# Performance work log

Measured on AMD Instinct MI355X. Metric: run time of the kernel, lower is better.

The kernel has to match this reference:

```python
import jax, jax.numpy as jnp
import numpy as np

RHO = 1060.0   # blood density kg/m^3
DX = 1e-3      # grid spacing
CCFL = 0.9     # CFL number
EPS_A = 1e-6   # area floor


def setup_inputs() -> dict:
    key = jax.random.key(0)
    k0, k1, k2 = jax.random.split(key, 3)
    M = 90000          # 3 vessels x 30000 cells
    T = 150            # time steps
    Rs = jax.random.normal(k0, (4,), dtype=jnp.float32)
    sim_dat = jnp.ones((2, M), dtype=jnp.float32)            # row0: A, row1: Q seed
    sim_dat_const = jax.random.uniform(k1, (11, M), dtype=jnp.float32)
    input_data = jax.random.uniform(k2, (T,), dtype=jnp.float32)
    strides = jnp.array([[0, 30000], [30000, 60000], [60000, 90000]], dtype=jnp.int32)
    return {"Rs": Rs, "sim_dat": sim_dat, "sim_dat_const": sim_dat_const,
            "input_data": input_data, "strides": strides, "upper": T}


def reference(Rs, sim_dat, sim_dat_const, input_data, strides, upper):
    M = sim_dat.shape[1]
    # --- SimDense: softplus reparam of 4 resistance scale factors ---
    rs = jax.nn.softplus(Rs)
    idx = jnp.arange(M)
    m1 = (idx >= strides[1, 0]) & (idx < strides[1, 1])  # vessel 1 region
    m2 = (idx >= strides[2, 0]) & (idx < strides[2, 1])  # vessel 2 region
    # constant rows (shifted positive)
    A0 = sim_dat_const[0] + 0.5     # reference area
    beta = sim_dat_const[1] + 1.0   # wall stiffness
    R1 = sim_dat_const[7] + 0.5     # proximal resistance (VAR_INDEX_1)
    R2 = sim_dat_const[8] + 0.5     # distal resistance (VAR_INDEX_2)
    # scatter scaled resistances into vessel-1 / vessel-2 regions
    R1 = jnp.where(m1, rs[0] * R1, jnp.where(m2, rs[2] * R1, R1))
    R2 = jnp.where(m1, rs[1] * R2, jnp.where(m2, rs[3] * R2, R2))
    Rtot = R1 + R2

    A_init = sim_dat[0]
    Q_init = 0.1 * sim_dat[1]
    starts = strides[:, 0]
    ends = strides[:, 1] - 1
    mids = (strides[:, 0] + strides[:, 1]) // 2

    def step(carry, inflow):
        A, Q = carry
        A = jnp.maximum(A, EPS_A)
        sq = jnp.sqrt(A / A0)
        P = beta * (sq - 1.0)                 # tube-law pressure
        u = Q / A
        c = jnp.sqrt(0.5 * beta / RHO * sq)   # wave speed
        smax = jnp.max(jnp.abs(u) + c)
        dt = CCFL * DX / smax                 # CFL-limited timestep
        # conservative fluxes for (A, Q)
        F_A = Q
        F_Q = Q * u + beta / (3.0 * RHO * A0) * A * sq
        # Lax-Friedrichs interface fluxes
        fhA = 0.5 * (F_A[:-1] + F_A[1:]) - 0.5 * smax * (A[1:] - A[:-1])
        fhQ = 0.5 * (F_Q[:-1] + F_Q[1:]) - 0.5 * smax * (Q[1:] - Q[:-1])
        lam = dt / DX
        A_new = A.at[1:-1].add(-lam * (fhA[1:] - fhA[:-1]))
        Q_new = Q.at[1:-1].add(-lam * (fhQ[1:] - fhQ[:-1]))
        # inlet / junction BC: prescribed inflow at each vessel start
        Q_new = Q_new.at[starts].set(inflow)
        # outlet BC: resistive Windkessel Q = P / (R1 + R2)
        Q_new = Q_new.at[ends].set(P[ends] / Rtot[ends])
        A_new = jnp.maximum(A_new, EPS_A)
        return (A_new, Q_new), P[mids]          # record mid-vessel pressures

    _, p = jax.lax.scan(step, (A_init, Q_init), input_data)
    return p  # [upper, 3]
```

## Files before the change

kernel.cpp:

```cpp
#include <hip/hip_runtime.h>

static constexpr int MM  = 90000;
static constexpr int TT  = 150;
static constexpr int BS  = 256;
static constexpr int CPT = 4;
static constexpr int CPB = BS * CPT;
static constexpr int NB  = (MM + CPB - 1) / CPB;
static constexpr int WPB = BS / 64;
static constexpr int NWAVE  = NB * WPB;
static constexpr int WPAGES = 384;
static constexpr int PAGE_U32 = 2048;
static constexpr int PAGE_U64 = 1024;

__device__ unsigned int       g_wmax[WPAGES][PAGE_U32];
__device__ unsigned long long g_edge_s[NB][PAGE_U64];
__device__ unsigned long long g_dummy64;

__device__ __forceinline__ float softplus_f(float x) {
    return fmaxf(x, 0.0f) + log1pf(expf(-fabsf(x)));
}
__device__ __forceinline__ unsigned long long packAQ(float A, float Q) {
    return ((unsigned long long)__float_as_uint(Q) << 32) | (unsigned long long)__float_as_uint(A);
}
#define AG_LOAD32(p)     __hip_atomic_load((p), __ATOMIC_RELAXED, __HIP_MEMORY_SCOPE_AGENT)
#define AG_LOAD64(p)     __hip_atomic_load((p), __ATOMIC_RELAXED, __HIP_MEMORY_SCOPE_AGENT)
#define AG_STORE32(p, v) __hip_atomic_store((p), (v), __ATOMIC_RELAXED, __HIP_MEMORY_SCOPE_AGENT)
#define AG_STORE64(p, v) __hip_atomic_store((p), (v), __ATOMIC_RELAXED, __HIP_MEMORY_SCOPE_AGENT)

#define DPP_MAX(x, ctrl, rm, bm)                                                     \
    x = fmaxf(x, __int_as_float(__builtin_amdgcn_update_dpp(                          \
                     0, __float_as_int(x), (ctrl), (rm), (bm), true)))
__device__ __forceinline__ float wave_max64(float x) {
    DPP_MAX(x, 0x111, 0xf, 0xf);
    DPP_MAX(x, 0x112, 0xf, 0xf);
    DPP_MAX(x, 0x114, 0xf, 0xe);
    DPP_MAX(x, 0x118, 0xf, 0xc);
    DPP_MAX(x, 0x142, 0xa, 0xf);
    DPP_MAX(x, 0x143, 0xc, 0xf);
    return x;
}

__global__ void init_ws_kernel() {
    int i = blockIdx.x * blockDim.x + threadIdx.x;
    int stride = gridDim.x * blockDim.x;
    unsigned int* pw = &g_wmax[0][0];
    for (int j = i; j < WPAGES * PAGE_U32; j += stride)
        pw[j] = ((j / PAGE_U32) < NWAVE) ? 0u : 1u;
    unsigned long long* pe = &g_edge_s[0][0];
    for (int j = i; j < NB * PAGE_U64; j += stride) pe[j] = 0ull;
    if (i == 0) g_dummy64 = ~0ull;
}

__global__ void __launch_bounds__(BS) sim_kernel(
    const float* __restrict__ Rs,
    const float* __restrict__ sim_dat,
    const float* __restrict__ sdc,
    const float* __restrict__ inflow,
    float* __restrict__ out)
{
    __shared__ float sE[2][WPB][2][3];
    __shared__ float s_bc[2];
    __shared__ float s_hL[3], s_hR[3];
    __shared__ float s_inflow[TT];

    const int b    = blockIdx.x;
    const int tid  = threadIdx.x;
    const int wv   = tid >> 6;
    const int lane = tid & 63;
    const int base = b * CPB + tid * CPT;
    const int gw   = b * WPB + wv;

    for (int j = tid; j < TT; j += BS) s_inflow[j] = inflow[j];

    float A[CPT], Q[CPT], A0v[CPT], bet[CPT], cbv[CPT], k2v[CPT], sq[CPT], FQ[CPT];
    bool  act[CPT];
    #pragma unroll
    for (int c = 0; c < CPT; ++c) {
        int i = base + c;
        act[c] = (i < MM);
        if (act[c]) {
            A[c]   = fmaxf(sim_dat[i], 1e-6f);
            Q[c]   = 0.1f * sim_dat[MM + i];
            A0v[c] = sdc[i] + 0.5f;
            bet[c] = sdc[MM + i] + 1.0f;
        } else { A[c] = 1.0f; Q[c] = 0.0f; A0v[c] = 1.0f; bet[c] = 1.0f; }
        cbv[c] = (0.5f * bet[c]) / 1060.0f;
        k2v[c] = bet[c] / (3180.0f * A0v[c]);
    }
    const bool isStart = (base == 0) | (base == 30000) | (base == 60000);
    const bool isEnd   = (base + 3 == 29999) | (base + 3 == 59999) | (base + 3 == 89999);
    const int midSlot = (base == 15000) ? 0 : (base == 45000) ? 1 : (base == 75000) ? 2 : -1;
    float Rtot = 1.0f;
    if (isEnd) {
        int i3 = base + 3;
        float R1 = sdc[7 * MM + i3] + 0.5f;
        float R2 = sdc[8 * MM + i3] + 0.5f;
        if (i3 == 59999)      { R1 *= softplus_f(Rs[0]); R2 *= softplus_f(Rs[1]); }
        else if (i3 == 89999) { R1 *= softplus_f(Rs[2]); R2 *= softplus_f(Rs[3]); }
        Rtot = R1 + R2;
    }

    const bool pubL = (tid == 0) && (b > 0);
    const bool pubR = (tid == BS - 1) && (b < NB - 1);

    const unsigned int* pwl = &g_wmax[lane][0];

    float s4 = 0.0f;
    #pragma unroll
    for (int c = 0; c < CPT; ++c) {
        sq[c] = sqrtf(A[c] / A0v[c]);
        float uu = Q[c] / A[c];
        float cc = sqrtf(cbv[c] * sq[c]);
        FQ[c] = Q[c] * uu + k2v[c] * A[c] * sq[c];
        s4 = fmaxf(s4, act[c] ? (fabsf(uu) + cc) : 0.0f);
    }
    if (pubL) {
        AG_STORE64(&g_edge_s[b][0], packAQ(A[0], Q[0]));
        AG_STORE64(&g_edge_s[b][1], (unsigned long long)__float_as_uint(FQ[0]));
    }
    if (pubR) {
        AG_STORE64(&g_edge_s[b][2], packAQ(A[3], Q[3]));
        AG_STORE64(&g_edge_s[b][3], (unsigned long long)__float_as_uint(FQ[3]));
    }
    {
        float red = wave_max64(s4);
        if (lane == 63) AG_STORE32(&g_wmax[gw][0], __float_as_uint(red));
    }
    if (lane == 0)       { sE[0][wv][0][0] = A[0]; sE[0][wv][0][1] = Q[0]; sE[0][wv][0][2] = FQ[0]; }
    else if (lane == 63) { sE[0][wv][1][0] = A[3]; sE[0][wv][1][1] = Q[3]; sE[0][wv][1][2] = FQ[3]; }

    for (int t = 0; t < TT; ++t) {
        const int par = t & 1, npar = par ^ 1;

        unsigned int x0, x1, x2, x3, x4, x5;
        unsigned long long e64;
        const unsigned long long* pE = &g_dummy64;
        if (wv == 0) {
            const int t4 = t * 4;
            if (lane == 0 && b > 0)           pE = &g_edge_s[b - 1][t4 + 2];
            else if (lane == 1 && b > 0)      pE = &g_edge_s[b - 1][t4 + 3];
            else if (lane == 2 && b < NB - 1) pE = &g_edge_s[b + 1][t4 + 0];
            else if (lane == 3 && b < NB - 1) pE = &g_edge_s[b + 1][t4 + 1];
            const unsigned int* p = pwl + t;
            x0 = AG_LOAD32(p);
            x1 = AG_LOAD32(p +  64 * PAGE_U32);
            x2 = AG_LOAD32(p + 128 * PAGE_U32);
            x3 = AG_LOAD32(p + 192 * PAGE_U32);
            x4 = AG_LOAD32(p + 256 * PAGE_U32);
            x5 = AG_LOAD32(p + 320 * PAGE_U32);
            e64 = AG_LOAD64(pE);
        }

        float Am = __shfl_up(A[3], 1, 64),  Qm = __shfl_up(Q[3], 1, 64),  Fm = __shfl_up(FQ[3], 1, 64);
        float Ap = __shfl_down(A[0], 1, 64), Qp = __shfl_down(Q[0], 1, 64), Fp = __shfl_down(FQ[0], 1, 64);

        float dFA[CPT], lapA[CPT], dFQ[CPT], lapQ[CPT];
        #pragma unroll
        for (int c = 0; c < CPT; ++c) {
            float Al = (c == 0) ? Am : A[c-1],  Ql = (c == 0) ? Qm : Q[c-1],  Fl = (c == 0) ? Fm : FQ[c-1];
            float Ar = (c == 3) ? Ap : A[c+1],  Qr = (c == 3) ? Qp : Q[c+1],  Fr = (c == 3) ? Fp : FQ[c+1];
            dFA[c]  = 0.5f * (Qr - Ql);
            lapA[c] = 0.5f * (Ar - 2.0f * A[c] + Al);
            dFQ[c]  = 0.5f * (Fr - Fl);
            lapQ[c] = 0.5f * (Qr - 2.0f * Q[c] + Ql);
        }
        if (midSlot >= 0) out[t * 3 + midSlot] = bet[0] * (sq[0] - 1.0f);
        float qFix = 0.0f;
        if (isStart) qFix = s_inflow[t];
        if (isEnd)   qFix = (bet[3] * (sq[3] - 1.0f)) / Rtot;

        if (wv == 0) {
            const unsigned int* p = pwl + t;
            bool ok = __all((x0 != 0u) & (x1 != 0u) & (x2 != 0u) & (x3 != 0u) &
                            (x4 != 0u) & (x5 != 0u) & (e64 != 0ull));
            while (!ok) {
                x0 = AG_LOAD32(p);
                x1 = AG_LOAD32(p +  64 * PAGE_U32);
                x2 = AG_LOAD32(p + 128 * PAGE_U32);
                x3 = AG_LOAD32(p + 192 * PAGE_U32);
                x4 = AG_LOAD32(p + 256 * PAGE_U32);
                x5 = AG_LOAD32(p + 320 * PAGE_U32);
                e64 = AG_LOAD64(pE);
                ok = __all((x0 != 0u) & (x1 != 0u) & (x2 != 0u) & (x3 != 0u) &
                           (x4 != 0u) & (x5 != 0u) & (e64 != 0ull));
            }
            if (lane == 0 && b > 0)           { s_hL[0] = __uint_as_float((unsigned int)e64);
                                                s_hL[1] = __uint_as_float((unsigned int)(e64 >> 32)); }
            else if (lane == 1 && b > 0)      { s_hL[2] = __uint_as_float((unsigned int)e64); }
            else if (lane == 2 && b < NB - 1) { s_hR[0] = __uint_as_float((unsigned int)e64);
                                                s_hR[1] = __uint_as_float((unsigned int)(e64 >> 32)); }
            else if (lane == 3 && b < NB - 1) { s_hR[2] = __uint_as_float((unsigned int)e64); }
            float m = fmaxf(fmaxf(fmaxf(__uint_as_float(x0), __uint_as_float(x1)),
                                  fmaxf(__uint_as_float(x2), __uint_as_float(x3))),
                            fmaxf(__uint_as_float(x4), __uint_as_float(x5)));
            m = wave_max64(m);
            const float smax = __int_as_float(__builtin_amdgcn_readlane(__float_as_int(m), 63));
            const float dt  = ((float)(0.9 * 0.001)) / smax;
            const float lam = dt / 0.001f;
            const float w   = lam * smax;
            if (lane == 0) { s_bc[0] = lam; s_bc[1] = w; }
        }
        __syncthreads();
        const float lam = s_bc[0];
        const float w   = s_bc[1];

        if (lane == 0 && (wv > 0 || b > 0)) {
            float Al, Ql, Fl;
            if (wv > 0) { Al = sE[par][wv-1][1][0]; Ql = sE[par][wv-1][1][1]; Fl = sE[par][wv-1][1][2]; }
            else        { Al = s_hL[0];             Ql = s_hL[1];             Fl = s_hL[2]; }
            dFA[0]  = 0.5f * (Q[1] - Ql);
            lapA[0] = 0.5f * (A[1] - 2.0f * A[0] + Al);
            dFQ[0]  = 0.5f * (FQ[1] - Fl);
            lapQ[0] = 0.5f * (Q[1] - 2.0f * Q[0] + Ql);
        }
        if (lane == 63 && (wv < WPB - 1 || b < NB - 1)) {
            float Ar, Qr, Fr;
            if (wv < WPB - 1) { Ar = sE[par][wv+1][0][0]; Qr = sE[par][wv+1][0][1]; Fr = sE[par][wv+1][0][2]; }
            else              { Ar = s_hR[0];             Qr = s_hR[1];             Fr = s_hR[2]; }
            dFA[3]  = 0.5f * (Qr - Q[2]);
            lapA[3] = 0.5f * (Ar - 2.0f * A[3] + A[2]);
            dFQ[3]  = 0.5f * (Fr - FQ[2]);
            lapQ[3] = 0.5f * (Qr - 2.0f * Q[3] + Q[2]);
        }

        #pragma unroll
        for (int c = 0; c < CPT; ++c) {
            int i = base + c;
            if (act[c] && i > 0 && i < MM - 1) {
                A[c] = fmaf(w, lapA[c], fmaf(-lam, dFA[c], A[c]));
                Q[c] = fmaf(w, lapQ[c], fmaf(-lam, dFQ[c], Q[c]));
            }
        }
        if (isStart) Q[0] = qFix;
        if (isEnd)   Q[3] = qFix;
        #pragma unroll
        for (int c = 0; c < CPT; ++c) A[c] = fmaxf(A[c], 1e-6f);

        const int n4 = (t + 1) * 4;
        if (pubL) AG_STORE64(&g_edge_s[b][n4 + 0], packAQ(A[0], Q[0]));
        if (pubR) AG_STORE64(&g_edge_s[b][n4 + 2], packAQ(A[3], Q[3]));

        float uu[CPT];
        s4 = 0.0f;
        #pragma unroll
        for (int c = 0; c < CPT; ++c) {
            sq[c] = sqrtf(A[c] / A0v[c]);
            uu[c] = Q[c] / A[c];
            float cc = sqrtf(cbv[c] * sq[c]);
            s4 = fmaxf(s4, act[c] ? (fabsf(uu[c]) + cc) : 0.0f);
        }
        {
            float red = wave_max64(s4);
            if (lane == 63) AG_STORE32(&g_wmax[gw][t + 1], __float_as_uint(red));
        }
        #pragma unroll
        for (int c = 0; c < CPT; ++c)
            FQ[c] = Q[c] * uu[c] + k2v[c] * A[c] * sq[c];

        if (pubL) AG_STORE64(&g_edge_s[b][n4 + 1], (unsigned long long)__float_as_uint(FQ[0]));
        if (pubR) AG_STORE64(&g_edge_s[b][n4 + 3], (unsigned long long)__float_as_uint(FQ[3]));

        if (lane == 0)       { sE[npar][wv][0][0] = A[0]; sE[npar][wv][0][1] = Q[0]; sE[npar][wv][0][2] = FQ[0]; }
        else if (lane == 63) { sE[npar][wv][1][0] = A[3]; sE[npar][wv][1][1] = Q[3]; sE[npar][wv][1][2] = FQ[3]; }
    }
}

extern "C" void kernel_launch(void* const* d_in, const int* in_sizes, int n_in,
                              void* d_out, int out_size, void* d_ws, size_t ws_size,
                              hipStream_t stream) {
    (void)in_sizes; (void)n_in; (void)d_ws; (void)ws_size; (void)out_size;

    const float* Rs      = (const float*)d_in[0];
    const float* sim_dat = (const float*)d_in[1];
    const float* sdc     = (const float*)d_in[2];
    const float* inflow  = (const float*)d_in[3];
    float* out = (float*)d_out;

    hipLaunchKernelGGL(init_ws_kernel, dim3(240), dim3(256), 0, stream);

    hipLaunchKernelGGL(sim_kernel, dim3(NB), dim3(BS), 0, stream,
                       Rs, sim_dat, sdc, inflow, out);
}
```

Baseline: 459.9 us.

## Replace block barrier with LDS flag broadcast and pack halo edges into dwordx4

```diff
diff --git a/kernel.cpp b/kernel.cpp
--- a/kernel.cpp
+++ b/kernel.cpp
@@ -7,28 +7,59 @@
 static constexpr int CPB = BS * CPT;
 static constexpr int NB  = (MM + CPB - 1) / CPB;
 static constexpr int WPB = BS / 64;
-static constexpr int NWAVE  = NB * WPB;
+static constexpr int NWAVE = NB * WPB;
 static constexpr int WPAGES = 384;
 static constexpr int PAGE_U32 = 2048;
-static constexpr int PAGE_U64 = 1024;
-
-__device__ unsigned int       g_wmax[WPAGES][PAGE_U32];
-__device__ unsigned long long g_edge_s[NB][PAGE_U64];
-__device__ unsigned long long g_dummy64;
+static constexpr int DUMMY_OFF = 1024;
+
+typedef unsigned int u32x4 __attribute__((ext_vector_type(4)));
+
+__device__ __attribute__((aligned(128))) unsigned int g_wmax[WPAGES][PAGE_U32];
+__device__ __attribute__((aligned(128))) unsigned int g_edge[NB][PAGE_U32];
 
 __device__ __forceinline__ float softplus_f(float x) {
     return fmaxf(x, 0.0f) + log1pf(expf(-fabsf(x)));
 }
-__device__ __forceinline__ unsigned long long packAQ(float A, float Q) {
-    return ((unsigned long long)__float_as_uint(Q) << 32) | (unsigned long long)__float_as_uint(A);
-}
-#define AG_LOAD32(p)     __hip_atomic_load((p), __ATOMIC_RELAXED, __HIP_MEMORY_SCOPE_AGENT)
-#define AG_LOAD64(p)     __hip_atomic_load((p), __ATOMIC_RELAXED, __HIP_MEMORY_SCOPE_AGENT)
 #define AG_STORE32(p, v) __hip_atomic_store((p), (v), __ATOMIC_RELAXED, __HIP_MEMORY_SCOPE_AGENT)
-#define AG_STORE64(p, v) __hip_atomic_store((p), (v), __ATOMIC_RELAXED, __HIP_MEMORY_SCOPE_AGENT)
-
-#define DPP_MAX(x, ctrl, rm, bm)                                                     \
-    x = fmaxf(x, __int_as_float(__builtin_amdgcn_update_dpp(                          \
+
+#define ISSUE7(x0,x1,x2,x3,x4,x5,h,p0,p1,p2,p3,p4,p5,ph)                        \
+    asm volatile("global_load_dword %0, %7, off sc1\n\t"                        \
+                 "global_load_dword %1, %8, off sc1\n\t"                        \
+                 "global_load_dword %2, %9, off sc1\n\t"                        \
+                 "global_load_dword %3, %10, off sc1\n\t"                       \
+                 "global_load_dword %4, %11, off sc1\n\t"                       \
+                 "global_load_dword %5, %12, off sc1\n\t"                       \
+                 "global_load_dwordx4 %6, %13, off sc1"                         \
+                 : "=&v"(x0),"=&v"(x1),"=&v"(x2),"=&v"(x3),"=&v"(x4),"=&v"(x5),"=&v"(h) \
+                 : "v"(p0),"v"(p1),"v"(p2),"v"(p3),"v"(p4),"v"(p5),"v"(ph)      \
+                 : "memory")
+#define POLL7(x0,x1,x2,x3,x4,x5,h,p0,p1,p2,p3,p4,p5,ph)                         \
+    asm volatile("global_load_dword %0, %7, off sc1\n\t"                        \
+                 "global_load_dword %1, %8, off sc1\n\t"                        \
+                 "global_load_dword %2, %9, off sc1\n\t"                        \
+                 "global_load_dword %3, %10, off sc1\n\t"                       \
+                 "global_load_dword %4, %11, off sc1\n\t"                       \
+                 "global_load_dword %5, %12, off sc1\n\t"                       \
+                 "global_load_dwordx4 %6, %13, off sc1\n\t"                     \
+                 "s_waitcnt vmcnt(0)"                                           \
+                 : "=&v"(x0),"=&v"(x1),"=&v"(x2),"=&v"(x3),"=&v"(x4),"=&v"(x5),"=&v"(h) \
+                 : "v"(p0),"v"(p1),"v"(p2),"v"(p3),"v"(p4),"v"(p5),"v"(ph)      \
+                 : "memory")
+#define ISSUE1(h, ph)                                                           \
+    asm volatile("global_load_dwordx4 %0, %1, off sc1"                          \
+                 : "=&v"(h) : "v"(ph) : "memory")
+#define POLL1(h, ph)                                                            \
+    asm volatile("global_load_dwordx4 %0, %1, off sc1\n\t"                      \
+                 "s_waitcnt vmcnt(0)"                                           \
+                 : "=&v"(h) : "v"(ph) : "memory")
+#define WAITVM()  do { asm volatile("s_waitcnt vmcnt(0)" ::: "memory");         \
+                       __builtin_amdgcn_sched_barrier(0); } while (0)
+#define FENCE_LDS() asm volatile("s_waitcnt lgkmcnt(0)" ::: "memory")
+#define STORE_X4(p, v)                                                          \
+    asm volatile("global_store_dwordx4 %0, %1, off sc1" :: "v"(p), "v"(v) : "memory")
+
+#define DPP_MAX(x, ctrl, rm, bm)                                                \
+    x = fmaxf(x, __int_as_float(__builtin_amdgcn_update_dpp(                    \
                      0, __float_as_int(x), (ctrl), (rm), (bm), true)))
 __device__ __forceinline__ float wave_max64(float x) {
     DPP_MAX(x, 0x111, 0xf, 0xf);
@@ -45,10 +76,9 @@
     int stride = gridDim.x * blockDim.x;
     unsigned int* pw = &g_wmax[0][0];
     for (int j = i; j < WPAGES * PAGE_U32; j += stride)
-        pw[j] = ((j / PAGE_U32) < NWAVE) ? 0u : 1u;
-    unsigned long long* pe = &g_edge_s[0][0];
-    for (int j = i; j < NB * PAGE_U64; j += stride) pe[j] = 0ull;
-    if (i == 0) g_dummy64 = ~0ull;
+        pw[j] = (((j >> 11) < NWAVE) && ((j & (PAGE_U32 - 1)) < DUMMY_OFF)) ? 0u : 1u;
+    unsigned int* pe = &g_edge[0][0];
+    for (int j = i; j < NB * PAGE_U32; j += stride) pe[j] = 0u;
 }
 
 __global__ void __launch_bounds__(BS) sim_kernel(
@@ -59,8 +89,7 @@
     float* __restrict__ out)
 {
     __shared__ float sE[2][WPB][2][3];
-    __shared__ float s_bc[2];
-    __shared__ float s_hL[3], s_hR[3];
+    __shared__ unsigned long long s_lamw[TT];
     __shared__ float s_inflow[TT];
 
     const int b    = blockIdx.x;
@@ -70,7 +99,7 @@
     const int base = b * CPB + tid * CPT;
     const int gw   = b * WPB + wv;
 
-    for (int j = tid; j < TT; j += BS) s_inflow[j] = inflow[j];
+    for (int j = tid; j < TT; j += BS) { s_inflow[j] = inflow[j]; s_lamw[j] = 0ull; }
 
     float A[CPT], Q[CPT], A0v[CPT], bet[CPT], cbv[CPT], k2v[CPT], sq[CPT], FQ[CPT];
     bool  act[CPT];
@@ -103,8 +132,6 @@
     const bool pubL = (tid == 0) && (b > 0);
     const bool pubR = (tid == BS - 1) && (b < NB - 1);
 
-    const unsigned int* pwl = &g_wmax[lane][0];
-
     float s4 = 0.0f;
     #pragma unroll
     for (int c = 0; c < CPT; ++c) {
@@ -114,41 +141,36 @@
         FQ[c] = Q[c] * uu + k2v[c] * A[c] * sq[c];
         s4 = fmaxf(s4, act[c] ? (fabsf(uu) + cc) : 0.0f);
     }
-    if (pubL) {
-        AG_STORE64(&g_edge_s[b][0], packAQ(A[0], Q[0]));
-        AG_STORE64(&g_edge_s[b][1], (unsigned long long)__float_as_uint(FQ[0]));
-    }
-    if (pubR) {
-        AG_STORE64(&g_edge_s[b][2], packAQ(A[3], Q[3]));
-        AG_STORE64(&g_edge_s[b][3], (unsigned long long)__float_as_uint(FQ[3]));
-    }
+    if (pubL) { u32x4 ev = { __float_as_uint(A[0]), __float_as_uint(Q[0]), __float_as_uint(FQ[0]), 0u };
+                STORE_X4(&g_edge[b][0], ev); }
+    if (pubR) { u32x4 ev = { __float_as_uint(A[3]), __float_as_uint(Q[3]), __float_as_uint(FQ[3]), 0u };
+                STORE_X4(&g_edge[b][4], ev); }
+    if (lane == 0)       { sE[0][wv][0][0] = A[0]; sE[0][wv][0][1] = Q[0]; sE[0][wv][0][2] = FQ[0]; }
+    else if (lane == 63) { sE[0][wv][1][0] = A[3]; sE[0][wv][1][1] = Q[3]; sE[0][wv][1][2] = FQ[3]; }
     {
         float red = wave_max64(s4);
+        FENCE_LDS();
         if (lane == 63) AG_STORE32(&g_wmax[gw][0], __float_as_uint(red));
     }
-    if (lane == 0)       { sE[0][wv][0][0] = A[0]; sE[0][wv][0][1] = Q[0]; sE[0][wv][0][2] = FQ[0]; }
-    else if (lane == 63) { sE[0][wv][1][0] = A[3]; sE[0][wv][1][1] = Q[3]; sE[0][wv][1][2] = FQ[3]; }
+    __syncthreads();
 
     for (int t = 0; t < TT; ++t) {
         const int par = t & 1, npar = par ^ 1;
 
         unsigned int x0, x1, x2, x3, x4, x5;
-        unsigned long long e64;
-        const unsigned long long* pE = &g_dummy64;
+        u32x4 h;
+        const unsigned int *p0, *p1, *p2, *p3, *p4, *p5, *ph;
         if (wv == 0) {
-            const int t4 = t * 4;
-            if (lane == 0 && b > 0)           pE = &g_edge_s[b - 1][t4 + 2];
-            else if (lane == 1 && b > 0)      pE = &g_edge_s[b - 1][t4 + 3];
-            else if (lane == 2 && b < NB - 1) pE = &g_edge_s[b + 1][t4 + 0];
-            else if (lane == 3 && b < NB - 1) pE = &g_edge_s[b + 1][t4 + 1];
-            const unsigned int* p = pwl + t;
-            x0 = AG_LOAD32(p);
-            x1 = AG_LOAD32(p +  64 * PAGE_U32);
-            x2 = AG_LOAD32(p + 128 * PAGE_U32);
-            x3 = AG_LOAD32(p + 192 * PAGE_U32);
-            x4 = AG_LOAD32(p + 256 * PAGE_U32);
-            x5 = AG_LOAD32(p + 320 * PAGE_U32);
-            e64 = AG_LOAD64(pE);
+            p0 = &g_wmax[lane      ][t];  p1 = &g_wmax[lane +  64][t];
+            p2 = &g_wmax[lane + 128][t];  p3 = &g_wmax[lane + 192][t];
+            p4 = &g_wmax[lane + 256][t];  p5 = &g_wmax[lane + 320][t];
+            ph = (lane == 0 && b > 0) ? &g_edge[b - 1][t * 8 + 4]
+                                      : &g_wmax[lane][DUMMY_OFF];
+            ISSUE7(x0, x1, x2, x3, x4, x5, h, p0, p1, p2, p3, p4, p5, ph);
+        } else if (wv == WPB - 1) {
+            ph = (lane == 63 && b < NB - 1) ? &g_edge[b + 1][t * 8]
+                                            : &g_wmax[lane][DUMMY_OFF];
+            ISSUE1(h, ph);
         }
 
         float Am = __shfl_up(A[3], 1, 64),  Qm = __shfl_up(Q[3], 1, 64),  Fm = __shfl_up(FQ[3], 1, 64);
@@ -164,50 +186,51 @@
             dFQ[c]  = 0.5f * (Fr - Fl);
             lapQ[c] = 0.5f * (Qr - 2.0f * Q[c] + Ql);
         }
-        if (midSlot >= 0) out[t * 3 + midSlot] = bet[0] * (sq[0] - 1.0f);
         float qFix = 0.0f;
         if (isStart) qFix = s_inflow[t];
         if (isEnd)   qFix = (bet[3] * (sq[3] - 1.0f)) / Rtot;
-
+        const float Pmid = bet[0] * (sq[0] - 1.0f);
+
+        float lam, w;
+        float hA = 0.0f, hQ = 0.0f, hF = 0.0f;
         if (wv == 0) {
-            const unsigned int* p = pwl + t;
-            bool ok = __all((x0 != 0u) & (x1 != 0u) & (x2 != 0u) & (x3 != 0u) &
-                            (x4 != 0u) & (x5 != 0u) & (e64 != 0ull));
-            while (!ok) {
-                x0 = AG_LOAD32(p);
-                x1 = AG_LOAD32(p +  64 * PAGE_U32);
-                x2 = AG_LOAD32(p + 128 * PAGE_U32);
-                x3 = AG_LOAD32(p + 192 * PAGE_U32);
-                x4 = AG_LOAD32(p + 256 * PAGE_U32);
-                x5 = AG_LOAD32(p + 320 * PAGE_U32);
-                e64 = AG_LOAD64(pE);
-                ok = __all((x0 != 0u) & (x1 != 0u) & (x2 != 0u) & (x3 != 0u) &
-                           (x4 != 0u) & (x5 != 0u) & (e64 != 0ull));
+            WAITVM();
+            while (!__all((x0 != 0u) & (x1 != 0u) & (x2 != 0u) & (x3 != 0u) &
+                          (x4 != 0u) & (x5 != 0u) & (h.x != 0u) & (h.z != 0u))) {
+                POLL7(x0, x1, x2, x3, x4, x5, h, p0, p1, p2, p3, p4, p5, ph);
             }
-            if (lane == 0 && b > 0)           { s_hL[0] = __uint_as_float((unsigned int)e64);
-                                                s_hL[1] = __uint_as_float((unsigned int)(e64 >> 32)); }
-            else if (lane == 1 && b > 0)      { s_hL[2] = __uint_as_float((unsigned int)e64); }
-            else if (lane == 2 && b < NB - 1) { s_hR[0] = __uint_as_float((unsigned int)e64);
-                                                s_hR[1] = __uint_as_float((unsigned int)(e64 >> 32)); }
-            else if (lane == 3 && b < NB - 1) { s_hR[2] = __uint_as_float((unsigned int)e64); }
+            hA = __uint_as_float(h.x); hQ = __uint_as_float(h.y); hF = __uint_as_float(h.z);
             float m = fmaxf(fmaxf(fmaxf(__uint_as_float(x0), __uint_as_float(x1)),
                                   fmaxf(__uint_as_float(x2), __uint_as_float(x3))),
                             fmaxf(__uint_as_float(x4), __uint_as_float(x5)));
             m = wave_max64(m);
             const float smax = __int_as_float(__builtin_amdgcn_readlane(__float_as_int(m), 63));
-            const float dt  = ((float)(0.9 * 0.001)) / smax;
-            const float lam = dt / 0.001f;
-            const float w   = lam * smax;
-            if (lane == 0) { s_bc[0] = lam; s_bc[1] = w; }
-        }
-        __syncthreads();
-        const float lam = s_bc[0];
-        const float w   = s_bc[1];
+            const float dt = ((float)(0.9 * 0.001)) / smax;
+            lam = dt / 0.001f;
+            w   = lam * smax;
+            if (lane == 0) {
+                unsigned long long v = ((unsigned long long)__float_as_uint(w) << 32)
+                                       | (unsigned long long)__float_as_uint(lam);
+                __hip_atomic_store(&s_lamw[t], v, __ATOMIC_RELEASE, __HIP_MEMORY_SCOPE_WORKGROUP);
+            }
+        } else {
+            if (wv == WPB - 1) {
+                WAITVM();
+                while (!__all((h.x != 0u) & (h.z != 0u))) { POLL1(h, ph); }
+                hA = __uint_as_float(h.x); hQ = __uint_as_float(h.y); hF = __uint_as_float(h.z);
+            }
+            unsigned long long lw;
+            do {
+                lw = __hip_atomic_load(&s_lamw[t], __ATOMIC_ACQUIRE, __HIP_MEMORY_SCOPE_WORKGROUP);
+            } while ((unsigned int)lw == 0u);
+            lam = __uint_as_float((unsigned int)lw);
+            w   = __uint_as_float((unsigned int)(lw >> 32));
+        }
 
         if (lane == 0 && (wv > 0 || b > 0)) {
             float Al, Ql, Fl;
             if (wv > 0) { Al = sE[par][wv-1][1][0]; Ql = sE[par][wv-1][1][1]; Fl = sE[par][wv-1][1][2]; }
-            else        { Al = s_hL[0];             Ql = s_hL[1];             Fl = s_hL[2]; }
+            else        { Al = hA;                  Ql = hQ;                  Fl = hF; }
             dFA[0]  = 0.5f * (Q[1] - Ql);
             lapA[0] = 0.5f * (A[1] - 2.0f * A[0] + Al);
             dFQ[0]  = 0.5f * (FQ[1] - Fl);
@@ -216,7 +239,7 @@
         if (lane == 63 && (wv < WPB - 1 || b < NB - 1)) {
             float Ar, Qr, Fr;
             if (wv < WPB - 1) { Ar = sE[par][wv+1][0][0]; Qr = sE[par][wv+1][0][1]; Fr = sE[par][wv+1][0][2]; }
-            else              { Ar = s_hR[0];             Qr = s_hR[1];             Fr = s_hR[2]; }
+            else              { Ar = hA;                  Qr = hQ;                  Fr = hF; }
             dFA[3]  = 0.5f * (Qr - Q[2]);
             lapA[3] = 0.5f * (Ar - 2.0f * A[3] + A[2]);
             dFQ[3]  = 0.5f * (Fr - FQ[2]);
@@ -235,10 +258,7 @@
         if (isEnd)   Q[3] = qFix;
         #pragma unroll
         for (int c = 0; c < CPT; ++c) A[c] = fmaxf(A[c], 1e-6f);
-
-        const int n4 = (t + 1) * 4;
-        if (pubL) AG_STORE64(&g_edge_s[b][n4 + 0], packAQ(A[0], Q[0]));
-        if (pubR) AG_STORE64(&g_edge_s[b][n4 + 2], packAQ(A[3], Q[3]));
+        if (midSlot >= 0) out[t * 3 + midSlot] = Pmid;
 
         float uu[CPT];
         s4 = 0.0f;
@@ -249,19 +269,23 @@
             float cc = sqrtf(cbv[c] * sq[c]);
             s4 = fmaxf(s4, act[c] ? (fabsf(uu[c]) + cc) : 0.0f);
         }
+        #pragma unroll
+        for (int c = 0; c < CPT; ++c)
+            FQ[c] = Q[c] * uu[c] + k2v[c] * A[c] * sq[c];
+
+        const int n8 = (t + 1) * 8;
+        if (pubL) { u32x4 ev = { __float_as_uint(A[0]), __float_as_uint(Q[0]), __float_as_uint(FQ[0]), 0u };
+                    STORE_X4(&g_edge[b][n8], ev); }
+        if (pubR) { u32x4 ev = { __float_as_uint(A[3]), __float_as_uint(Q[3]), __float_as_uint(FQ[3]), 0u };
+                    STORE_X4(&g_edge[b][n8 + 4], ev); }
+
+        if (lane == 0)       { sE[npar][wv][0][0] = A[0]; sE[npar][wv][0][1] = Q[0]; sE[npar][wv][0][2] = FQ[0]; }
+        else if (lane == 63) { sE[npar][wv][1][0] = A[3]; sE[npar][wv][1][1] = Q[3]; sE[npar][wv][1][2] = FQ[3]; }
         {
             float red = wave_max64(s4);
+            FENCE_LDS();
             if (lane == 63) AG_STORE32(&g_wmax[gw][t + 1], __float_as_uint(red));
         }
-        #pragma unroll
-        for (int c = 0; c < CPT; ++c)
-            FQ[c] = Q[c] * uu[c] + k2v[c] * A[c] * sq[c];
-
-        if (pubL) AG_STORE64(&g_edge_s[b][n4 + 1], (unsigned long long)__float_as_uint(FQ[0]));
-        if (pubR) AG_STORE64(&g_edge_s[b][n4 + 3], (unsigned long long)__float_as_uint(FQ[3]));
-
-        if (lane == 0)       { sE[npar][wv][0][0] = A[0]; sE[npar][wv][0][1] = Q[0]; sE[npar][wv][0][2] = FQ[0]; }
-        else if (lane == 63) { sE[npar][wv][1][0] = A[3]; sE[npar][wv][1][1] = Q[3]; sE[npar][wv][1][2] = FQ[3]; }
     }
 }
 
```

Result: slower. 655.8 us (+42.6%).

## Replicate simulation per XCD and centralize CFL max reduction through leader block

Applied to the files above, without the earlier changes.

```diff
diff --git a/kernel.cpp b/kernel.cpp
--- a/kernel.cpp
+++ b/kernel.cpp
@@ -5,16 +5,21 @@
 static constexpr int BS  = 256;
 static constexpr int CPT = 4;
 static constexpr int CPB = BS * CPT;
-static constexpr int NB  = (MM + CPB - 1) / CPB;
+static constexpr int NBR = (MM + CPB - 1) / CPB;
 static constexpr int WPB = BS / 64;
-static constexpr int NWAVE  = NB * WPB;
-static constexpr int WPAGES = 384;
-static constexpr int PAGE_U32 = 2048;
-static constexpr int PAGE_U64 = 1024;
-
-__device__ unsigned int       g_wmax[WPAGES][PAGE_U32];
-__device__ unsigned long long g_edge_s[NB][PAGE_U64];
-__device__ unsigned long long g_dummy64;
+static constexpr int NXCD = 8;
+static constexpr int NLAUNCH = NBR * NXCD;
+static constexpr int PG32 = 512;
+static constexpr int PG64 = 1024;
+static constexpr int GUARD_MAX = 1 << 16;
+
+typedef unsigned int u32x2 __attribute__((ext_vector_type(2)));
+
+__device__ __attribute__((aligned(128))) unsigned int       g_bmax[NXCD][128][PG32];
+__device__ __attribute__((aligned(128))) unsigned int       g_res [NXCD][128][PG32];
+__device__ __attribute__((aligned(128))) unsigned long long g_edge[NXCD][NBR][PG64];
+__device__ int          g_cnt[NXCD];
+__device__ unsigned int g_done;
 
 __device__ __forceinline__ float softplus_f(float x) {
     return fmaxf(x, 0.0f) + log1pf(expf(-fabsf(x)));
@@ -22,13 +27,29 @@
 __device__ __forceinline__ unsigned long long packAQ(float A, float Q) {
     return ((unsigned long long)__float_as_uint(Q) << 32) | (unsigned long long)__float_as_uint(A);
 }
-#define AG_LOAD32(p)     __hip_atomic_load((p), __ATOMIC_RELAXED, __HIP_MEMORY_SCOPE_AGENT)
-#define AG_LOAD64(p)     __hip_atomic_load((p), __ATOMIC_RELAXED, __HIP_MEMORY_SCOPE_AGENT)
-#define AG_STORE32(p, v) __hip_atomic_store((p), (v), __ATOMIC_RELAXED, __HIP_MEMORY_SCOPE_AGENT)
-#define AG_STORE64(p, v) __hip_atomic_store((p), (v), __ATOMIC_RELAXED, __HIP_MEMORY_SCOPE_AGENT)
-
-#define DPP_MAX(x, ctrl, rm, bm)                                                     \
-    x = fmaxf(x, __int_as_float(__builtin_amdgcn_update_dpp(                          \
+
+#define DSTORE32(p, v) asm volatile("global_store_dword %0, %1, off\n\t"            \
+                                    "global_store_dword %0, %1, off sc1"            \
+                                    :: "v"(p), "v"(v) : "memory")
+#define DSTORE64(p, v) asm volatile("global_store_dwordx2 %0, %1, off\n\t"          \
+                                    "global_store_dwordx2 %0, %1, off sc1"          \
+                                    :: "v"(p), "v"(v) : "memory")
+#define SLD32(d, p) asm volatile("global_load_dword %0, %1, off sc1\n\t"            \
+                                 "s_waitcnt vmcnt(0)" : "=&v"(d) : "v"(p) : "memory")
+#define SLD64(d, p) asm volatile("global_load_dwordx2 %0, %1, off sc1\n\t"          \
+                                 "s_waitcnt vmcnt(0)" : "=&v"(d) : "v"(p) : "memory")
+#define SC1_LD32(d, p) asm volatile("global_load_dword %0, %1, off sc1\n\ts_waitcnt vmcnt(0)" \
+                                    : "=v"(d) : "v"(p) : "memory")
+#define SC1_ST32(p, v) asm volatile("global_store_dword %0, %1, off sc1\n\ts_waitcnt vmcnt(0)" \
+                                    :: "v"(p), "v"(v) : "memory")
+
+#define LOC_ADD32(p, z) __hip_atomic_fetch_add((unsigned int*)(p), (z), \
+                            __ATOMIC_RELAXED, __HIP_MEMORY_SCOPE_WORKGROUP)
+#define LOC_ADD64(p, z) __hip_atomic_fetch_add((unsigned long long*)(p), (z), \
+                            __ATOMIC_RELAXED, __HIP_MEMORY_SCOPE_WORKGROUP)
+
+#define DPP_MAX(x, ctrl, rm, bm)                                                \
+    x = fmaxf(x, __int_as_float(__builtin_amdgcn_update_dpp(                    \
                      0, __float_as_int(x), (ctrl), (rm), (bm), true)))
 __device__ __forceinline__ float wave_max64(float x) {
     DPP_MAX(x, 0x111, 0xf, 0xf);
@@ -43,15 +64,19 @@
 __global__ void init_ws_kernel() {
     int i = blockIdx.x * blockDim.x + threadIdx.x;
     int stride = gridDim.x * blockDim.x;
-    unsigned int* pw = &g_wmax[0][0];
-    for (int j = i; j < WPAGES * PAGE_U32; j += stride)
-        pw[j] = ((j / PAGE_U32) < NWAVE) ? 0u : 1u;
-    unsigned long long* pe = &g_edge_s[0][0];
-    for (int j = i; j < NB * PAGE_U64; j += stride) pe[j] = 0ull;
-    if (i == 0) g_dummy64 = ~0ull;
-}
-
-__global__ void __launch_bounds__(BS) sim_kernel(
+    unsigned int* pb = &g_bmax[0][0][0];
+    for (int j = i; j < NXCD * 128 * PG32; j += stride) pb[j] = 0u;
+    unsigned int* ps = &g_res[0][0][0];
+    for (int j = i; j < NXCD * 128 * PG32; j += stride) ps[j] = 0u;
+    unsigned long long* pe = &g_edge[0][0][0];
+    for (int j = i; j < NXCD * NBR * PG64; j += stride) pe[j] = 0ull;
+    if (i == 0) {
+        g_done = 0u;
+        for (int r = 0; r < NXCD; ++r) g_cnt[r] = 0;
+    }
+}
+
+__global__ void __launch_bounds__(BS, 4) sim_kernel(
     const float* __restrict__ Rs,
     const float* __restrict__ sim_dat,
     const float* __restrict__ sdc,
@@ -59,18 +84,55 @@
     float* __restrict__ out)
 {
     __shared__ float sE[2][WPB][2][3];
+    __shared__ float s_redf[TT + 1][WPB];
+    __shared__ float s_inflow[TT];
     __shared__ float s_bc[2];
     __shared__ float s_hL[3], s_hR[3];
-    __shared__ float s_inflow[TT];
-
-    const int b    = blockIdx.x;
+    __shared__ int   s_panic;
+    __shared__ int   s_slot, s_rep, s_go;
+
     const int tid  = threadIdx.x;
     const int wv   = tid >> 6;
     const int lane = tid & 63;
-    const int base = b * CPB + tid * CPT;
-    const int gw   = b * WPB + wv;
+
+    if (tid == 0) {
+        unsigned int xcc;
+        asm volatile("s_getreg_b32 %0, hwreg(HW_REG_XCC_ID)" : "=s"(xcc));
+        const int rep = (int)(xcc & 7u);
+        s_rep  = rep;
+        s_slot = atomicAdd(&g_cnt[rep], 1);
+    }
+    __syncthreads();
+    const int slot = s_slot;
+    const int rep  = s_rep;
+    if (slot >= NBR) return;
+
+    if (tid == 0) {
+        int go = 1;
+        for (;;) {
+            unsigned int c, d;
+            SC1_LD32(c, (const unsigned int*)&g_cnt[rep]);
+            if ((int)c >= NBR) break;
+            SC1_LD32(d, &g_done);
+            if (d != 0u) { go = 0; break; }
+            __builtin_amdgcn_s_sleep(64);
+        }
+        s_go = go;
+    }
+    __syncthreads();
+    if (!s_go) return;
 
     for (int j = tid; j < TT; j += BS) s_inflow[j] = inflow[j];
+    for (int j = tid; j < (TT + 1) * WPB; j += BS) (&s_redf[0][0])[j] = 0.0f;
+    if (tid == 0) s_panic = 0;
+    __syncthreads();
+
+    unsigned int zo_;
+    asm volatile("v_mov_b32 %0, 0" : "=v"(zo_));
+    const unsigned int       zo   = zo_;
+    const unsigned long long zo64 = zo_;
+
+    const int base = slot * CPB + tid * CPT;
 
     float A[CPT], Q[CPT], A0v[CPT], bet[CPT], cbv[CPT], k2v[CPT], sq[CPT], FQ[CPT];
     bool  act[CPT];
@@ -100,10 +162,9 @@
         Rtot = R1 + R2;
     }
 
-    const bool pubL = (tid == 0) && (b > 0);
-    const bool pubR = (tid == BS - 1) && (b < NB - 1);
-
-    const unsigned int* pwl = &g_wmax[lane][0];
+    const bool pubL = (tid == 0) && (slot > 0);
+    const bool pubR = (tid == BS - 1) && (slot < NBR - 1);
+    const bool isLeader = (slot == 0);
 
     float s4 = 0.0f;
     #pragma unroll
@@ -114,42 +175,35 @@
         FQ[c] = Q[c] * uu + k2v[c] * A[c] * sq[c];
         s4 = fmaxf(s4, act[c] ? (fabsf(uu) + cc) : 0.0f);
     }
-    if (pubL) {
-        AG_STORE64(&g_edge_s[b][0], packAQ(A[0], Q[0]));
-        AG_STORE64(&g_edge_s[b][1], (unsigned long long)__float_as_uint(FQ[0]));
-    }
-    if (pubR) {
-        AG_STORE64(&g_edge_s[b][2], packAQ(A[3], Q[3]));
-        AG_STORE64(&g_edge_s[b][3], (unsigned long long)__float_as_uint(FQ[3]));
-    }
+    if (pubL) { unsigned long long v = packAQ(A[0], Q[0]);
+                u32x2 e0 = { (unsigned int)v, (unsigned int)(v >> 32) };
+                u32x2 e1 = { __float_as_uint(FQ[0]), 0u };
+                DSTORE64(&g_edge[rep][slot][0], e0);
+                DSTORE64(&g_edge[rep][slot][1], e1); }
+    if (pubR) { unsigned long long v = packAQ(A[3], Q[3]);
+                u32x2 e0 = { (unsigned int)v, (unsigned int)(v >> 32) };
+                u32x2 e1 = { __float_as_uint(FQ[3]), 0u };
+                DSTORE64(&g_edge[rep][slot][2], e0);
+                DSTORE64(&g_edge[rep][slot][3], e1); }
+    if (lane == 0)       { sE[0][wv][0][0] = A[0]; sE[0][wv][0][1] = Q[0]; sE[0][wv][0][2] = FQ[0]; }
+    else if (lane == 63) { sE[0][wv][1][0] = A[3]; sE[0][wv][1][1] = Q[3]; sE[0][wv][1][2] = FQ[3]; }
     {
         float red = wave_max64(s4);
-        if (lane == 63) AG_STORE32(&g_wmax[gw][0], __float_as_uint(red));
-    }
-    if (lane == 0)       { sE[0][wv][0][0] = A[0]; sE[0][wv][0][1] = Q[0]; sE[0][wv][0][2] = FQ[0]; }
-    else if (lane == 63) { sE[0][wv][1][0] = A[3]; sE[0][wv][1][1] = Q[3]; sE[0][wv][1][2] = FQ[3]; }
+        if (lane == 63) {
+            s_redf[0][wv] = red;
+            if (wv == 0) {
+                volatile float* sf = &s_redf[0][0];
+                int g2 = 0; float r1, r2, r3;
+                do { r1 = sf[1]; r2 = sf[2]; r3 = sf[3]; ++g2; }
+                while ((r1 == 0.0f || r2 == 0.0f || r3 == 0.0f) && g2 < GUARD_MAX);
+                float bm = fmaxf(fmaxf(red, r1), fmaxf(r2, r3));
+                DSTORE32(&g_bmax[rep][slot][0], __float_as_uint(bm));
+            }
+        }
+    }
 
     for (int t = 0; t < TT; ++t) {
         const int par = t & 1, npar = par ^ 1;
-
-        unsigned int x0, x1, x2, x3, x4, x5;
-        unsigned long long e64;
-        const unsigned long long* pE = &g_dummy64;
-        if (wv == 0) {
-            const int t4 = t * 4;
-            if (lane == 0 && b > 0)           pE = &g_edge_s[b - 1][t4 + 2];
-            else if (lane == 1 && b > 0)      pE = &g_edge_s[b - 1][t4 + 3];
-            else if (lane == 2 && b < NB - 1) pE = &g_edge_s[b + 1][t4 + 0];
-            else if (lane == 3 && b < NB - 1) pE = &g_edge_s[b + 1][t4 + 1];
-            const unsigned int* p = pwl + t;
-            x0 = AG_LOAD32(p);
-            x1 = AG_LOAD32(p +  64 * PAGE_U32);
-            x2 = AG_LOAD32(p + 128 * PAGE_U32);
-            x3 = AG_LOAD32(p + 192 * PAGE_U32);
-            x4 = AG_LOAD32(p + 256 * PAGE_U32);
-            x5 = AG_LOAD32(p + 320 * PAGE_U32);
-            e64 = AG_LOAD64(pE);
-        }
 
         float Am = __shfl_up(A[3], 1, 64),  Qm = __shfl_up(Q[3], 1, 64),  Fm = __shfl_up(FQ[3], 1, 64);
         float Ap = __shfl_down(A[0], 1, 64), Qp = __shfl_down(Q[0], 1, 64), Fp = __shfl_down(FQ[0], 1, 64);
@@ -170,41 +224,75 @@
         if (isEnd)   qFix = (bet[3] * (sq[3] - 1.0f)) / Rtot;
 
         if (wv == 0) {
-            const unsigned int* p = pwl + t;
-            bool ok = __all((x0 != 0u) & (x1 != 0u) & (x2 != 0u) & (x3 != 0u) &
-                            (x4 != 0u) & (x5 != 0u) & (e64 != 0ull));
-            while (!ok) {
-                x0 = AG_LOAD32(p);
-                x1 = AG_LOAD32(p +  64 * PAGE_U32);
-                x2 = AG_LOAD32(p + 128 * PAGE_U32);
-                x3 = AG_LOAD32(p + 192 * PAGE_U32);
-                x4 = AG_LOAD32(p + 256 * PAGE_U32);
-                x5 = AG_LOAD32(p + 320 * PAGE_U32);
-                e64 = AG_LOAD64(pE);
-                ok = __all((x0 != 0u) & (x1 != 0u) & (x2 != 0u) & (x3 != 0u) &
-                           (x4 != 0u) & (x5 != 0u) & (e64 != 0ull));
-            }
-            if (lane == 0 && b > 0)           { s_hL[0] = __uint_as_float((unsigned int)e64);
-                                                s_hL[1] = __uint_as_float((unsigned int)(e64 >> 32)); }
-            else if (lane == 1 && b > 0)      { s_hL[2] = __uint_as_float((unsigned int)e64); }
-            else if (lane == 2 && b < NB - 1) { s_hR[0] = __uint_as_float((unsigned int)e64);
-                                                s_hR[1] = __uint_as_float((unsigned int)(e64 >> 32)); }
-            else if (lane == 3 && b < NB - 1) { s_hR[2] = __uint_as_float((unsigned int)e64); }
-            float m = fmaxf(fmaxf(fmaxf(__uint_as_float(x0), __uint_as_float(x1)),
-                                  fmaxf(__uint_as_float(x2), __uint_as_float(x3))),
-                            fmaxf(__uint_as_float(x4), __uint_as_float(x5)));
-            m = wave_max64(m);
-            const float smax = __int_as_float(__builtin_amdgcn_readlane(__float_as_int(m), 63));
-            const float dt  = ((float)(0.9 * 0.001)) / smax;
+            const int t4 = t * 4;
+            const unsigned int *pA = nullptr, *pB = nullptr;
+            const unsigned long long *pC = nullptr;
+            bool hasA = false, hasB = false, hasC = false;
+            if (isLeader) {
+                hasA = true;  pA = &g_bmax[rep][lane][t];
+                hasB = (lane < NBR - 64);
+                if (hasB) pB = &g_bmax[rep][64 + lane][t];
+                if (lane == 24)      { hasC = true; pC = &g_edge[rep][1][t4 + 0]; }
+                else if (lane == 25) { hasC = true; pC = &g_edge[rep][1][t4 + 1]; }
+            } else {
+                if (lane == 0) { hasA = true; pA = &g_res[rep][slot][t]; }
+                if (lane == 0)                       { hasC = true; pC = &g_edge[rep][slot - 1][t4 + 2]; }
+                else if (lane == 1)                  { hasC = true; pC = &g_edge[rep][slot - 1][t4 + 3]; }
+                else if (lane == 2 && slot < NBR - 1){ hasC = true; pC = &g_edge[rep][slot + 1][t4 + 0]; }
+                else if (lane == 3 && slot < NBR - 1){ hasC = true; pC = &g_edge[rep][slot + 1][t4 + 1]; }
+            }
+            unsigned int ra = 1u, rb = 1u;
+            unsigned long long rc = 1ull;
+            int it = 0, guard = 0;
+            for (;;) {
+                if ((++it & 3) != 0) {
+                    if (hasA) ra = LOC_ADD32(pA, zo);
+                    if (hasB) rb = LOC_ADD32(pB, zo);
+                    if (hasC) rc = LOC_ADD64(pC, zo64);
+                } else {
+                    if (hasA) SLD32(ra, pA);
+                    if (hasB) SLD32(rb, pB);
+                    if (hasC) { u32x2 tmp; SLD64(tmp, pC);
+                                rc = ((unsigned long long)tmp.y << 32) | tmp.x; }
+                }
+                if (__all((ra != 0u) & (rb != 0u) & ((unsigned int)rc != 0u))) break;
+                if (++guard >= GUARD_MAX) break;
+            }
+            float smaxv;
+            if (isLeader) {
+                float vA = __uint_as_float(ra);
+                float vB = hasB ? __uint_as_float(rb) : 0.0f;
+                float m = wave_max64(fmaxf(vA, vB));
+                smaxv = __int_as_float(__builtin_amdgcn_readlane(__float_as_int(m), 63));
+                const unsigned int sb = __float_as_uint(smaxv);
+                DSTORE32(&g_res[rep][lane][t], sb);
+                if (lane < NBR - 64) DSTORE32(&g_res[rep][64 + lane][t], sb);
+                if (lane == 24)      { s_hR[0] = __uint_as_float((unsigned int)rc);
+                                       s_hR[1] = __uint_as_float((unsigned int)(rc >> 32)); }
+                else if (lane == 25) { s_hR[2] = __uint_as_float((unsigned int)rc); }
+            } else {
+                smaxv = __int_as_float(__builtin_amdgcn_readlane((int)ra, 0));
+                if (lane == 0)                        { s_hL[0] = __uint_as_float((unsigned int)rc);
+                                                        s_hL[1] = __uint_as_float((unsigned int)(rc >> 32)); }
+                else if (lane == 1)                   { s_hL[2] = __uint_as_float((unsigned int)rc); }
+                else if (lane == 2 && slot < NBR - 1) { s_hR[0] = __uint_as_float((unsigned int)rc);
+                                                        s_hR[1] = __uint_as_float((unsigned int)(rc >> 32)); }
+                else if (lane == 3 && slot < NBR - 1) { s_hR[2] = __uint_as_float((unsigned int)rc); }
+            }
+            const float dt  = ((float)(0.9 * 0.001)) / smaxv;
             const float lam = dt / 0.001f;
-            const float w   = lam * smax;
-            if (lane == 0) { s_bc[0] = lam; s_bc[1] = w; }
+            const float w   = lam * smaxv;
+            if (lane == 0) {
+                s_bc[0] = lam; s_bc[1] = w;
+                if (guard >= GUARD_MAX) s_panic = 1;
+            }
         }
         __syncthreads();
+        if (s_panic) break;
         const float lam = s_bc[0];
         const float w   = s_bc[1];
 
-        if (lane == 0 && (wv > 0 || b > 0)) {
+        if (lane == 0 && (wv > 0 || slot > 0)) {
             float Al, Ql, Fl;
             if (wv > 0) { Al = sE[par][wv-1][1][0]; Ql = sE[par][wv-1][1][1]; Fl = sE[par][wv-1][1][2]; }
             else        { Al = s_hL[0];             Ql = s_hL[1];             Fl = s_hL[2]; }
@@ -213,7 +301,7 @@
             dFQ[0]  = 0.5f * (FQ[1] - Fl);
             lapQ[0] = 0.5f * (Q[1] - 2.0f * Q[0] + Ql);
         }
-        if (lane == 63 && (wv < WPB - 1 || b < NB - 1)) {
+        if (lane == 63 && (wv < WPB - 1 || slot < NBR - 1)) {
             float Ar, Qr, Fr;
             if (wv < WPB - 1) { Ar = sE[par][wv+1][0][0]; Qr = sE[par][wv+1][0][1]; Fr = sE[par][wv+1][0][2]; }
             else              { Ar = s_hR[0];             Qr = s_hR[1];             Fr = s_hR[2]; }
@@ -237,8 +325,12 @@
         for (int c = 0; c < CPT; ++c) A[c] = fmaxf(A[c], 1e-6f);
 
         const int n4 = (t + 1) * 4;
-        if (pubL) AG_STORE64(&g_edge_s[b][n4 + 0], packAQ(A[0], Q[0]));
-        if (pubR) AG_STORE64(&g_edge_s[b][n4 + 2], packAQ(A[3], Q[3]));
+        if (pubL) { unsigned long long v = packAQ(A[0], Q[0]);
+                    u32x2 e0 = { (unsigned int)v, (unsigned int)(v >> 32) };
+                    DSTORE64(&g_edge[rep][slot][n4 + 0], e0); }
+        if (pubR) { unsigned long long v = packAQ(A[3], Q[3]);
+                    u32x2 e0 = { (unsigned int)v, (unsigned int)(v >> 32) };
+                    DSTORE64(&g_edge[rep][slot][n4 + 2], e0); }
 
         float uu[CPT];
         s4 = 0.0f;
@@ -249,20 +341,34 @@
             float cc = sqrtf(cbv[c] * sq[c]);
             s4 = fmaxf(s4, act[c] ? (fabsf(uu[c]) + cc) : 0.0f);
         }
+        FQ[0] = Q[0] * uu[0] + k2v[0] * A[0] * sq[0];
+        FQ[3] = Q[3] * uu[3] + k2v[3] * A[3] * sq[3];
+        if (pubL) { u32x2 e1 = { __float_as_uint(FQ[0]), 0u };
+                    DSTORE64(&g_edge[rep][slot][n4 + 1], e1); }
+        if (pubR) { u32x2 e1 = { __float_as_uint(FQ[3]), 0u };
+                    DSTORE64(&g_edge[rep][slot][n4 + 3], e1); }
+        FQ[1] = Q[1] * uu[1] + k2v[1] * A[1] * sq[1];
+        FQ[2] = Q[2] * uu[2] + k2v[2] * A[2] * sq[2];
+
         {
             float red = wave_max64(s4);
-            if (lane == 63) AG_STORE32(&g_wmax[gw][t + 1], __float_as_uint(red));
-        }
-        #pragma unroll
-        for (int c = 0; c < CPT; ++c)
-            FQ[c] = Q[c] * uu[c] + k2v[c] * A[c] * sq[c];
-
-        if (pubL) AG_STORE64(&g_edge_s[b][n4 + 1], (unsigned long long)__float_as_uint(FQ[0]));
-        if (pubR) AG_STORE64(&g_edge_s[b][n4 + 3], (unsigned long long)__float_as_uint(FQ[3]));
-
+            if (lane == 63) {
+                s_redf[t + 1][wv] = red;
+                if (wv == 0) {
+                    volatile float* sf = &s_redf[t + 1][0];
+                    int g2 = 0; float r1, r2, r3;
+                    do { r1 = sf[1]; r2 = sf[2]; r3 = sf[3]; ++g2; }
+                    while ((r1 == 0.0f || r2 == 0.0f || r3 == 0.0f) && g2 < GUARD_MAX);
+                    float bm = fmaxf(fmaxf(red, r1), fmaxf(r2, r3));
+                    DSTORE32(&g_bmax[rep][slot][t + 1], __float_as_uint(bm));
+                }
+            }
+        }
         if (lane == 0)       { sE[npar][wv][0][0] = A[0]; sE[npar][wv][0][1] = Q[0]; sE[npar][wv][0][2] = FQ[0]; }
         else if (lane == 63) { sE[npar][wv][1][0] = A[3]; sE[npar][wv][1][1] = Q[3]; sE[npar][wv][1][2] = FQ[3]; }
     }
+
+    if (slot == 0 && tid == 0) SC1_ST32(&g_done, 1u);
 }
 
 extern "C" void kernel_launch(void* const* d_in, const int* in_sizes, int n_in,
@@ -278,6 +384,6 @@
 
     hipLaunchKernelGGL(init_ws_kernel, dim3(240), dim3(256), 0, stream);
 
-    hipLaunchKernelGGL(sim_kernel, dim3(NB), dim3(BS), 0, stream,
+    hipLaunchKernelGGL(sim_kernel, dim3(NLAUNCH), dim3(BS), 0, stream,
                        Rs, sim_dat, sdc, inflow, out);
 }
```

New measurement: 898.9 us. 1.95x slower.
